# Kernel tuning notes

Hardware: AMD Instinct MI355X
Metric: run time of the kernel (lower is better)

## Reference

```python
import jax, jax.numpy as jnp
import numpy as np

B, T, C = 4, 2048, 768
H, D = 6, 128


def apply_rotary_emb(x, cos, sin):
    # x: (B, T, H, D); cos, sin: (1, T, 1, D//2)
    d = x.shape[-1] // 2
    x1, x2 = x[..., :d], x[..., d:]
    y1 = x1 * cos + x2 * sin
    y2 = -x1 * sin + x2 * cos
    return jnp.concatenate([y1, y2], axis=-1)


def rmsnorm(x):
    eps = 1e-15
    ms = jnp.mean(x * x, axis=-1, keepdims=True)
    return x / jnp.sqrt(ms + eps)


def setup_inputs() -> dict:
    key = jax.random.key(0)
    ks = jax.random.split(key, 7)
    s = 0.02
    return {
        "x": jax.random.normal(ks[0], (B, T, C), jnp.float32),
        "cos": jax.random.normal(ks[1], (1, T, 1, D // 2), jnp.float32),
        "sin": jax.random.normal(ks[2], (1, T, 1, D // 2), jnp.float32),
        "Wq": jax.random.normal(ks[3], (C, C), jnp.float32) * s,
        "Wk": jax.random.normal(ks[4], (C, C), jnp.float32) * s,
        "Wv": jax.random.normal(ks[5], (C, C), jnp.float32) * s,
        "Wo": jax.random.normal(ks[6], (C, C), jnp.float32) * s,
    }


def reference(x, cos, sin, Wq, Wk, Wv, Wo):
    b, t, c = x.shape
    # QKV projections (nn.Linear: x @ W.T)
    q = (x @ Wq.T).reshape(b, t, H, D)
    k = (x @ Wk.T).reshape(b, t, H, D)
    v = (x @ Wv.T).reshape(b, t, H, D)
    # RoPE then QK-RMSNorm
    q = rmsnorm(apply_rotary_emb(q, cos, sin))
    k = rmsnorm(apply_rotary_emb(k, cos, sin))
    # (B, H, T, D)
    q = q.transpose(0, 2, 1, 3)
    k = k.transpose(0, 2, 1, 3)
    v = v.transpose(0, 2, 1, 3)
    scores = jnp.einsum('bhqd,bhkd->bhqk', q, k) / jnp.sqrt(jnp.float32(D))
    causal = jnp.tril(jnp.ones((t, t), dtype=bool))
    scores = jnp.where(causal[None, None], scores, -jnp.inf)
    attn = jax.nn.softmax(scores, axis=-1)
    out = jnp.einsum('bhqk,bhkd->bhqd', attn, v)
    out = out.transpose(0, 2, 1, 3).reshape(b, t, c)
    return out @ Wo.T
```

## Files before the change

kernel.cpp:

```cpp
#include <hip/hip_runtime.h>

#define T_SEQ 2048
#define NH    6
#define HD    128
#define CDIM  768
#define NQKV  2304
#define MROWS 8192
#define NSLOT 1104

typedef __attribute__((ext_vector_type(8)))  short bf16x8;
typedef __attribute__((ext_vector_type(4)))  float f32x4;
typedef __attribute__((ext_vector_type(16))) float f32x16;
typedef __attribute__((ext_vector_type(2)))  int   i32x2;

__device__ __forceinline__ unsigned short f2bf(float f){
  unsigned int u = __builtin_bit_cast(unsigned int, f);
  u += 0x7fffu + ((u >> 16) & 1u);
  return (unsigned short)(u >> 16);
}
__device__ __forceinline__ float bf2f(unsigned short h){
  unsigned int u = ((unsigned int)h) << 16;
  return __builtin_bit_cast(float, u);
}
__device__ __forceinline__ unsigned int cvtpk(float lo, float hi){
  unsigned int r;
  asm("v_cvt_pk_bf16_f32 %0, %1, %2" : "=v"(r) : "v"(lo), "v"(hi));
  return r;
}

__device__ __forceinline__ void gload_lds16(const void* g, void* l){
  __builtin_amdgcn_global_load_lds(
      (const __attribute__((address_space(1))) unsigned int*)g,
      (__attribute__((address_space(3))) unsigned int*)l, 16, 0, 0);
}

__device__ __forceinline__ int ncq(int Q){
  return Q < 3 ? 1 : Q < 7 ? 2 : Q < 10 ? 3 : Q < 14 ? 4 : 5;
}
__device__ __forceinline__ int cumc(int Q){
  return Q < 4 ? Q : Q < 8 ? 3 + 2*(Q-3) : Q < 11 ? 11 + 3*(Q-7)
       : Q < 15 ? 20 + 4*(Q-10) : 36 + 5*(Q-14);
}

__global__ __launch_bounds__(256) void cvt_f32_bf16(
    const float* __restrict__ in, unsigned short* __restrict__ out, int n4){
  int i = blockIdx.x * 256 + threadIdx.x;
  if (i >= n4) return;
  float4 v = reinterpret_cast<const float4*>(in)[i];
  ushort4 o;
  o.x = f2bf(v.x); o.y = f2bf(v.y); o.z = f2bf(v.z); o.w = f2bf(v.w);
  reinterpret_cast<ushort4*>(out)[i] = o;
}

__global__ __launch_bounds__(256) void cvt_w4(
    const float* __restrict__ w0, const float* __restrict__ w1,
    const float* __restrict__ w2, const float* __restrict__ w3,
    unsigned short* __restrict__ out){
  const int which = blockIdx.y;
  const float* src = which == 0 ? w0 : which == 1 ? w1 : which == 2 ? w2 : w3;
  int i = blockIdx.x * 256 + threadIdx.x;
  float4 v = reinterpret_cast<const float4*>(src)[i];
  ushort4 o;
  o.x = f2bf(v.x); o.y = f2bf(v.y); o.z = f2bf(v.z); o.w = f2bf(v.w);
  reinterpret_cast<ushort4*>(out + (size_t)which * CDIM * CDIM)[i] = o;
}

template<int EPI>
__global__ __launch_bounds__(256) void gemm_bt(
    const unsigned short* __restrict__ A,
    const unsigned short* __restrict__ B,
    void* __restrict__ Cv, int M, int N, int K,
    const float* __restrict__ cosp, const float* __restrict__ sinp)
{
  __shared__ unsigned short As[128 * 64];
  __shared__ unsigned short Bs[128 * 64];
  const int tid  = threadIdx.x;
  const int lane = tid & 63;
  const int wave = tid >> 6;
  const int lr = lane & 15, lg = lane >> 4;
  const int srow = lane >> 3;
  const int sslot = (lane & 7) ^ (lane >> 3);
  const int gx = gridDim.x, gy = gridDim.y, nwg = gx * gy;
  const int flat = blockIdx.y * gx + blockIdx.x;
  const int nf = (flat & 7) * (nwg >> 3) + (flat >> 3);
  const int row0 = (nf / gy) * 128, col0 = (nf % gy) * 128;
  const int wrow = wave * 32;

  f32x4 acc[2][8];
  const f32x4 z = {0.f, 0.f, 0.f, 0.f};
  #pragma unroll
  for (int i = 0; i < 2; ++i)
    #pragma unroll
    for (int j = 0; j < 8; ++j) acc[i][j] = z;

  for (int k0 = 0; k0 < K; k0 += 64){
    #pragma unroll
    for (int i = 0; i < 4; ++i){
      int seg = wave * 4 + i;
      int r = seg * 8 + srow;
      gload_lds16(&A[(size_t)(row0 + r) * K + k0 + sslot * 8], &As[seg * 512]);
      gload_lds16(&B[(size_t)(col0 + r) * K + k0 + sslot * 8], &Bs[seg * 512]);
    }
    __syncthreads();
    #pragma unroll
    for (int kk = 0; kk < 64; kk += 32){
      bf16x8 af[2], bfr[8];
      #pragma unroll
      for (int mi = 0; mi < 2; ++mi)
        af[mi] = *reinterpret_cast<const bf16x8*>(
            &As[(wrow + mi*16 + lr) * 64 + ((((kk>>3) + lg) ^ (lr & 7)) * 8)]);
      #pragma unroll
      for (int ni = 0; ni < 8; ++ni)
        bfr[ni] = *reinterpret_cast<const bf16x8*>(
            &Bs[(ni*16 + lr) * 64 + ((((kk>>3) + lg) ^ (lr & 7)) * 8)]);
      #pragma unroll
      for (int mi = 0; mi < 2; ++mi)
        #pragma unroll
        for (int ni = 0; ni < 8; ++ni)
          acc[mi][ni] = __builtin_amdgcn_mfma_f32_16x16x32_bf16(af[mi], bfr[ni], acc[mi][ni], 0, 0, 0);
    }
    __syncthreads();
  }

  if (EPI == 0){
    float* Cf = reinterpret_cast<float*>(Cv);
    #pragma unroll
    for (int mi = 0; mi < 2; ++mi)
      #pragma unroll
      for (int ni = 0; ni < 8; ++ni)
        #pragma unroll
        for (int r = 0; r < 4; ++r)
          Cf[(size_t)(row0 + wrow + mi*16 + lg*4 + r) * N + col0 + ni*16 + lr] = acc[mi][ni][r];
  } else {
    unsigned short* Cb = reinterpret_cast<unsigned short*>(Cv);
    const int ct = col0 >> 7;
    if (ct >= 12){
      #pragma unroll
      for (int mi = 0; mi < 2; ++mi)
        #pragma unroll
        for (int ni = 0; ni < 8; ++ni)
          #pragma unroll
          for (int r = 0; r < 4; ++r)
            Cb[(size_t)(row0 + wrow + mi*16 + lg*4 + r) * N + col0 + ni*16 + lr] =
                f2bf(acc[mi][ni][r]);
    } else {
      #pragma unroll
      for (int mi = 0; mi < 2; ++mi){
        #pragma unroll
        for (int r = 0; r < 4; ++r){
          const int row = row0 + wrow + mi*16 + lg*4 + r;
          const int t = row & (T_SEQ - 1);
          float y1[4], y2[4], ssp = 0.f;
          #pragma unroll
          for (int ni = 0; ni < 4; ++ni){
            const int d = ni*16 + lr;
            float c = cosp[t * 64 + d];
            float s = sinp[t * 64 + d];
            float x1 = acc[mi][ni][r], x2 = acc[mi][ni+4][r];
            y1[ni] = x1 * c + x2 * s;
            y2[ni] = x2 * c - x1 * s;
            ssp += y1[ni]*y1[ni] + y2[ni]*y2[ni];
          }
          #pragma unroll
          for (int off = 1; off < 16; off <<= 1) ssp += __shfl_xor(ssp, off);
          const float inv = rsqrtf(ssp * (1.0f / 128.0f) + 1e-15f);
          #pragma unroll
          for (int ni = 0; ni < 4; ++ni){
            const int d = ni*16 + lr;
            Cb[(size_t)row * N + col0 + d]      = f2bf(y1[ni] * inv);
            Cb[(size_t)row * N + col0 + d + 64] = f2bf(y2[ni] * inv);
          }
        }
      }
    }
  }
}

__global__ __launch_bounds__(256) void transpose_v(
    const unsigned short* __restrict__ QKVb, unsigned short* __restrict__ Vt)
{
  __shared__ unsigned short tile[64][66];
  const int tid = threadIdx.x;
  const int t0  = blockIdx.x * 64;
  const int hd  = blockIdx.y;
  const int b   = blockIdx.z;
  const int h = hd >> 1, dhalf = (hd & 1) * 64;
  const unsigned short* src = QKVb + (size_t)b * T_SEQ * NQKV + 2 * CDIM + h * HD + dhalf;
  #pragma unroll
  for (int it = 0; it < 2; ++it){
    int ch = tid + it * 256;
    int r = ch >> 3, cc = (ch & 7) * 8;
    *reinterpret_cast<int4*>(&tile[r][cc]) =
        *reinterpret_cast<const int4*>(&src[(size_t)(t0 + r) * NQKV + cc]);
  }
  __syncthreads();
  unsigned short* dst = Vt + ((size_t)(b * NH + h) * HD + dhalf) * T_SEQ + t0;
  #pragma unroll
  for (int it = 0; it < 2; ++it){
    int ch = tid + it * 256;
    int d = ch >> 3, cc = (ch & 7) * 8;
    union { int4 v; unsigned short u[8]; } w;
    #pragma unroll
    for (int j = 0; j < 8; ++j) w.u[j] = tile[cc + j][d];
    *reinterpret_cast<int4*>(&dst[(size_t)d * T_SEQ + cc]) = w.v;
  }
}

__global__ __launch_bounds__(256) void attn_fwd(
    const unsigned short* __restrict__ QKVb,
    const unsigned short* __restrict__ Vt,
    unsigned short* __restrict__ AO,
    unsigned short* __restrict__ Op, float* __restrict__ Mp, float* __restrict__ Lp)
{
  __shared__ unsigned short Ks[64][136];
  __shared__ unsigned short Vs[128][72];
  const int tid = threadIdx.x;
  const int lane = tid & 63, wave = tid >> 6;
  const int l31 = lane & 31, hi = lane >> 5;

  const int flat = blockIdx.x;
  const int nf = (flat & 7) * 138 + (flat >> 3);
  const int bh = nf / 46;
  const int L = 45 - (nf % 46);
  int Q, c;
  if (L < 3)      { Q = L; c = 0; }
  else if (L < 11){ int m = L - 3;  Q = 3 + (m >> 1);  c = m & 1; }
  else if (L < 20){ int m = L - 11; Q = 7 + m / 3;     c = m % 3; }
  else if (L < 36){ int m = L - 20; Q = 10 + (m >> 2); c = m & 3; }
  else            { int m = L - 36; Q = 14 + m / 5;    c = m % 5; }
  const int nc = ncq(Q);
  const int tiles = 2 * Q + 2;
  const int base = tiles / nc, rem = tiles % nc;
  const int tbeg = c * base + (c < rem ? c : rem);
  const int tend = tbeg + base + (c < rem ? 1 : 0);
  const int b = bh / NH, h = bh % NH;
  const int qw = Q * 128 + wave * 32;

  const unsigned short* Qp = QKVb + (size_t)(b * T_SEQ) * NQKV + h * HD;
  const unsigned short* Kp = QKVb + (size_t)(b * T_SEQ) * NQKV + CDIM + h * HD;
  const unsigned short* Vp = Vt + (size_t)bh * HD * T_SEQ;

  bf16x8 qf[8];
  #pragma unroll
  for (int c4 = 0; c4 < 8; ++c4)
    qf[c4] = *reinterpret_cast<const bf16x8*>(
        &Qp[(size_t)(qw + l31) * NQKV + c4 * 16 + hi * 8]);

  f32x16 o[4];
  #pragma unroll
  for (int db = 0; db < 4; ++db)
    #pragma unroll
    for (int r = 0; r < 16; ++r) o[db][r] = 0.f;
  float mrun = -__builtin_inff(), lrun = 0.f;
  const float scl = 0.08838834764831845f;

  for (int t = tbeg; t < tend; ++t){
    const int kv0 = t * 64;
    #pragma unroll
    for (int it = 0; it < 4; ++it){
      int ch = tid + it * 256;
      int r = ch >> 4, cc = (ch & 15) * 8;
      *reinterpret_cast<int4*>(&Ks[r][cc]) =
          *reinterpret_cast<const int4*>(&Kp[(size_t)(kv0 + r) * NQKV + cc]);
      int rv = ch >> 3, cv = (ch & 7) * 8;
      *reinterpret_cast<int4*>(&Vs[rv][cv]) =
          *reinterpret_cast<const int4*>(&Vp[(size_t)rv * T_SEQ + kv0 + cv]);
    }
    __syncthreads();

    if (kv0 <= qw + 31){
      f32x16 s[2];
      #pragma unroll
      for (int r = 0; r < 16; ++r){ s[0][r] = 0.f; s[1][r] = 0.f; }
      __builtin_amdgcn_s_setprio(1);
      #pragma unroll
      for (int c4 = 0; c4 < 8; ++c4){
        bf16x8 k0 = *reinterpret_cast<const bf16x8*>(&Ks[l31][c4 * 16 + hi * 8]);
        bf16x8 k1 = *reinterpret_cast<const bf16x8*>(&Ks[32 + l31][c4 * 16 + hi * 8]);
        s[0] = __builtin_amdgcn_mfma_f32_32x32x16_bf16(k0, qf[c4], s[0], 0, 0, 0);
        s[1] = __builtin_amdgcn_mfma_f32_32x32x16_bf16(k1, qf[c4], s[1], 0, 0, 0);
      }
      __builtin_amdgcn_s_setprio(0);

      const int qg = qw + l31;
      if (kv0 + 63 > qw){
        #pragma unroll
        for (int blk = 0; blk < 2; ++blk)
          #pragma unroll
          for (int r = 0; r < 16; ++r){
            int kg = kv0 + 32 * blk + (r & 3) + 8 * (r >> 2) + 4 * hi;
            s[blk][r] = (kg <= qg) ? s[blk][r] * scl : -__builtin_inff();
          }
      } else {
        #pragma unroll
        for (int blk = 0; blk < 2; ++blk)
          #pragma unroll
          for (int r = 0; r < 16; ++r) s[blk][r] *= scl;
      }

      float t8[8];
      #pragma unroll
      for (int blk = 0; blk < 2; ++blk)
        #pragma unroll
        for (int j = 0; j < 4; ++j)
          t8[blk * 4 + j] = fmaxf(fmaxf(s[blk][4*j], s[blk][4*j+1]),
                                  fmaxf(s[blk][4*j+2], s[blk][4*j+3]));
      float pm = fmaxf(fmaxf(fmaxf(t8[0], t8[1]), fmaxf(t8[2], t8[3])),
                       fmaxf(fmaxf(t8[4], t8[5]), fmaxf(t8[6], t8[7])));
      pm = fmaxf(pm, __shfl_xor(pm, 32));

      if (__any(pm > mrun)){
        float mn = fmaxf(mrun, pm);
        float scf = (mrun == -__builtin_inff()) ? 0.f : __expf(mrun - mn);
        mrun = mn; lrun *= scf;
        #pragma unroll
        for (int r = 0; r < 16; ++r){
          float scr = __shfl(scf, (r & 3) + 8 * (r >> 2) + 4 * hi, 32);
          #pragma unroll
          for (int db = 0; db < 4; ++db) o[db][r] *= scr;
        }
      }

      float a8[8];
      #pragma unroll
      for (int blk = 0; blk < 2; ++blk)
        #pragma unroll
        for (int j = 0; j < 4; ++j){
          float p0 = __expf(s[blk][4*j]   - mrun);
          float p1 = __expf(s[blk][4*j+1] - mrun);
          float p2 = __expf(s[blk][4*j+2] - mrun);
          float p3 = __expf(s[blk][4*j+3] - mrun);
          s[blk][4*j] = p0; s[blk][4*j+1] = p1; s[blk][4*j+2] = p2; s[blk][4*j+3] = p3;
          a8[blk * 4 + j] = (p0 + p1) + (p2 + p3);
        }
      float ls = ((a8[0] + a8[1]) + (a8[2] + a8[3])) + ((a8[4] + a8[5]) + (a8[6] + a8[7]));
      lrun += ls + __shfl_xor(ls, 32);

      __builtin_amdgcn_s_setprio(1);
      #pragma unroll
      for (int kc = 0; kc < 4; ++kc){
        const int blk = kc >> 1, base2 = (kc & 1) * 8;
        unsigned int a0 = cvtpk(s[blk][base2+0], s[blk][base2+1]);
        unsigned int b0 = cvtpk(s[blk][base2+4], s[blk][base2+5]);
        unsigned int a1 = cvtpk(s[blk][base2+2], s[blk][base2+3]);
        unsigned int b1 = cvtpk(s[blk][base2+6], s[blk][base2+7]);
        i32x2 sw0 = __builtin_amdgcn_permlane32_swap((int)a0, (int)b0, false, false);
        i32x2 sw1 = __builtin_amdgcn_permlane32_swap((int)a1, (int)b1, false, false);
        union { bf16x8 v; unsigned int u[4]; } pa;
        pa.u[0] = (unsigned int)sw0[0];
        pa.u[1] = (unsigned int)sw1[0];
        pa.u[2] = (unsigned int)sw0[1];
        pa.u[3] = (unsigned int)sw1[1];
        #pragma unroll
        for (int db = 0; db < 4; ++db){
          bf16x8 vf = *reinterpret_cast<const bf16x8*>(
              &Vs[db * 32 + l31][kc * 16 + hi * 8]);
          o[db] = __builtin_amdgcn_mfma_f32_32x32x16_bf16(pa.v, vf, o[db], 0, 0, 0);
        }
      }
      __builtin_amdgcn_s_setprio(0);
    }
    __syncthreads();
  }

  if (nc == 1){
    float inv = 1.0f / lrun;
    #pragma unroll
    for (int r = 0; r < 16; ++r){
      const int crow = (r & 3) + 8 * (r >> 2) + 4 * hi;
      float ir = __shfl(inv, crow, 32);
      #pragma unroll
      for (int db = 0; db < 4; ++db)
        AO[((size_t)b * T_SEQ + qw + crow) * CDIM + h * HD + db * 32 + l31] =
            f2bf(o[db][r] * ir);
    }
  } else {
    const int slot = bh * 46 + cumc(Q) + c;
    unsigned short* OpW = Op + (size_t)slot * 128 * 128;
    #pragma unroll
    for (int r = 0; r < 16; ++r){
      const int row = wave * 32 + (r & 3) + 8 * (r >> 2) + 4 * hi;
      #pragma unroll
      for (int db = 0; db < 4; ++db)
        OpW[row * 128 + db * 32 + l31] = f2bf(o[db][r]);
    }
    if (hi == 0){
      Mp[(size_t)slot * 128 + wave * 32 + l31] = mrun;
      Lp[(size_t)slot * 128 + wave * 32 + l31] = lrun;
    }
  }
}

__global__ __launch_bounds__(256) void attn_combine(
    const unsigned short* __restrict__ Op, const float* __restrict__ Mp,
    const float* __restrict__ Lp, unsigned short* __restrict__ AO)
{
  const int Q  = 3 + blockIdx.x;
  const int bh = blockIdx.y;
  const int b = bh / NH, h = bh % NH;
  const int nc = ncq(Q);
  const int slot0 = bh * 46 + cumc(Q);
  #pragma unroll
  for (int u = 0; u < 16; ++u){
    int unit = threadIdx.x + u * 256;
    int r = unit >> 5, d4 = unit & 31;
    float m = -__builtin_inff();
    for (int cc = 0; cc < nc; ++cc)
      m = fmaxf(m, Mp[(size_t)(slot0 + cc) * 128 + r]);
    float l = 0.f;
    float a0 = 0.f, a1 = 0.f, a2 = 0.f, a3 = 0.f;
    for (int cc = 0; cc < nc; ++cc){
      float w = __expf(Mp[(size_t)(slot0 + cc) * 128 + r] - m);
      l += w * Lp[(size_t)(slot0 + cc) * 128 + r];
      const ushort4 v = *reinterpret_cast<const ushort4*>(
          &Op[((size_t)(slot0 + cc) * 128 + r) * 128 + d4 * 4]);
      a0 += w * bf2f(v.x); a1 += w * bf2f(v.y);
      a2 += w * bf2f(v.z); a3 += w * bf2f(v.w);
    }
    float inv = 1.0f / l;
    ushort4 ov;
    ov.x = f2bf(a0 * inv); ov.y = f2bf(a1 * inv);
    ov.z = f2bf(a2 * inv); ov.w = f2bf(a3 * inv);
    *reinterpret_cast<ushort4*>(
        &AO[((size_t)b * T_SEQ + Q * 128 + r) * CDIM + h * HD + d4 * 4]) = ov;
  }
}

extern "C" void kernel_launch(void* const* d_in, const int* in_sizes, int n_in,
                              void* d_out, int out_size, void* d_ws, size_t ws_size,
                              hipStream_t stream)
{
  (void)in_sizes; (void)n_in; (void)out_size; (void)ws_size;
  const float* x    = (const float*)d_in[0];
  const float* cosp = (const float*)d_in[1];
  const float* sinp = (const float*)d_in[2];
  const float* Wq   = (const float*)d_in[3];
  const float* Wk   = (const float*)d_in[4];
  const float* Wv   = (const float*)d_in[5];
  const float* Wo   = (const float*)d_in[6];
  float* out = (float*)d_out;

  unsigned short* xb    = (unsigned short*)d_ws;
  unsigned short* Wqkvb = xb    + (size_t)MROWS * CDIM;
  unsigned short* Wob   = Wqkvb + (size_t)NQKV * CDIM;
  unsigned short* QKVb  = Wob   + (size_t)CDIM * CDIM;
  unsigned short* Vtb   = QKVb  + (size_t)MROWS * NQKV;
  unsigned short* AO    = Vtb   + (size_t)MROWS * CDIM;
  unsigned short* Op    = AO    + (size_t)MROWS * CDIM;
  float* Mp = (float*)(Op + (size_t)NSLOT * 128 * 128);
  float* Lp = Mp + (size_t)NSLOT * 128;

  int n4x = MROWS * CDIM / 4;
  cvt_f32_bf16<<<(n4x + 255) / 256, 256, 0, stream>>>(x, xb, n4x);
  cvt_w4<<<dim3(CDIM * CDIM / 4 / 256, 4), 256, 0, stream>>>(Wq, Wk, Wv, Wo, Wqkvb);

  gemm_bt<1><<<dim3(MROWS / 128, NQKV / 128), 256, 0, stream>>>(
      xb, Wqkvb, QKVb, MROWS, NQKV, CDIM, cosp, sinp);
  transpose_v<<<dim3(T_SEQ / 64, 12, 4), 256, 0, stream>>>(QKVb, Vtb);
  attn_fwd<<<NSLOT, 256, 0, stream>>>(QKVb, Vtb, AO, Op, Mp, Lp);
  attn_combine<<<dim3(13, 24), 256, 0, stream>>>(Op, Mp, Lp, AO);
  gemm_bt<0><<<dim3(MROWS / 128, CDIM / 128), 256, 0, stream>>>(
      AO, Wob, out, MROWS, CDIM, CDIM, nullptr, nullptr);
}
```

Before: 214.5 us.

## Shrink attention query tile to 64 rows with 2-wave blocks and re-split schedule

Halves the attention query block from 128 to 64 rows, using 128-thread blocks (two waves) instead of four, and rebuilds the causal split-KV schedule with 90 work units per head and 2160 blocks. The aim is finer granularity and better load balance and occupancy across CUs, with less wasted work on the diagonal. In exchange, each K/V tile loaded into shared memory serves half as many query rows, so K/V traffic roughly doubles, and the combine kernel has more partial slots to merge.

```diff
diff --git a/kernel.cpp b/kernel.cpp
--- a/kernel.cpp
+++ b/kernel.cpp
@@ -6,7 +6,7 @@
 #define CDIM  768
 #define NQKV  2304
 #define MROWS 8192
-#define NSLOT 1104
+#define NSLOT 2160
 
 typedef __attribute__((ext_vector_type(8)))  short bf16x8;
 typedef __attribute__((ext_vector_type(4)))  float f32x4;
@@ -34,12 +34,12 @@
       (__attribute__((address_space(3))) unsigned int*)l, 16, 0, 0);
 }
 
-__device__ __forceinline__ int ncq(int Q){
-  return Q < 3 ? 1 : Q < 7 ? 2 : Q < 10 ? 3 : Q < 14 ? 4 : 5;
-}
-__device__ __forceinline__ int cumc(int Q){
-  return Q < 4 ? Q : Q < 8 ? 3 + 2*(Q-3) : Q < 11 ? 11 + 3*(Q-7)
-       : Q < 15 ? 20 + 4*(Q-10) : 36 + 5*(Q-14);
+__device__ __forceinline__ int ncq(int q){
+  return q < 7 ? 1 : q < 14 ? 2 : q < 21 ? 3 : q < 28 ? 4 : 5;
+}
+__device__ __forceinline__ int cumc(int q){
+  return q < 7 ? q : q < 14 ? 7 + 2*(q-7) : q < 21 ? 21 + 3*(q-14)
+       : q < 28 ? 42 + 4*(q-21) : 70 + 5*(q-28);
 }
 
 __global__ __launch_bounds__(256) void cvt_f32_bf16(
@@ -206,7 +206,7 @@
   }
 }
 
-__global__ __launch_bounds__(256) void attn_fwd(
+__global__ __launch_bounds__(128) void attn_fwd(
     const unsigned short* __restrict__ QKVb,
     const unsigned short* __restrict__ Vt,
     unsigned short* __restrict__ AO,
@@ -219,22 +219,22 @@
   const int l31 = lane & 31, hi = lane >> 5;
 
   const int flat = blockIdx.x;
-  const int nf = (flat & 7) * 138 + (flat >> 3);
-  const int bh = nf / 46;
-  const int L = 45 - (nf % 46);
-  int Q, c;
-  if (L < 3)      { Q = L; c = 0; }
-  else if (L < 11){ int m = L - 3;  Q = 3 + (m >> 1);  c = m & 1; }
-  else if (L < 20){ int m = L - 11; Q = 7 + m / 3;     c = m % 3; }
-  else if (L < 36){ int m = L - 20; Q = 10 + (m >> 2); c = m & 3; }
-  else            { int m = L - 36; Q = 14 + m / 5;    c = m % 5; }
-  const int nc = ncq(Q);
-  const int tiles = 2 * Q + 2;
+  const int nf = (flat & 7) * 270 + (flat >> 3);
+  const int bh = nf / 90;
+  const int L = 89 - (nf % 90);
+  int q, c;
+  if (L < 7)      { q = L; c = 0; }
+  else if (L < 21){ int m = L - 7;  q = 7 + (m >> 1);  c = m & 1; }
+  else if (L < 42){ int m = L - 21; q = 14 + m / 3;    c = m % 3; }
+  else if (L < 70){ int m = L - 42; q = 21 + (m >> 2); c = m & 3; }
+  else            { int m = L - 70; q = 28 + m / 5;    c = m % 5; }
+  const int nc = ncq(q);
+  const int tiles = q + 1;
   const int base = tiles / nc, rem = tiles % nc;
   const int tbeg = c * base + (c < rem ? c : rem);
   const int tend = tbeg + base + (c < rem ? 1 : 0);
   const int b = bh / NH, h = bh % NH;
-  const int qw = Q * 128 + wave * 32;
+  const int qw = q * 64 + wave * 32;
 
   const unsigned short* Qp = QKVb + (size_t)(b * T_SEQ) * NQKV + h * HD;
   const unsigned short* Kp = QKVb + (size_t)(b * T_SEQ) * NQKV + CDIM + h * HD;
@@ -257,8 +257,8 @@
   for (int t = tbeg; t < tend; ++t){
     const int kv0 = t * 64;
     #pragma unroll
-    for (int it = 0; it < 4; ++it){
-      int ch = tid + it * 256;
+    for (int it = 0; it < 8; ++it){
+      int ch = tid + it * 128;
       int r = ch >> 4, cc = (ch & 15) * 8;
       *reinterpret_cast<int4*>(&Ks[r][cc]) =
           *reinterpret_cast<const int4*>(&Kp[(size_t)(kv0 + r) * NQKV + cc]);
@@ -375,8 +375,8 @@
             f2bf(o[db][r] * ir);
     }
   } else {
-    const int slot = bh * 46 + cumc(Q) + c;
-    unsigned short* OpW = Op + (size_t)slot * 128 * 128;
+    const int slot = bh * 90 + cumc(q) + c;
+    unsigned short* OpW = Op + (size_t)slot * 64 * 128;
     #pragma unroll
     for (int r = 0; r < 16; ++r){
       const int row = wave * 32 + (r & 3) + 8 * (r >> 2) + 4 * hi;
@@ -385,8 +385,8 @@
         OpW[row * 128 + db * 32 + l31] = f2bf(o[db][r]);
     }
     if (hi == 0){
-      Mp[(size_t)slot * 128 + wave * 32 + l31] = mrun;
-      Lp[(size_t)slot * 128 + wave * 32 + l31] = lrun;
+      Mp[(size_t)slot * 64 + wave * 32 + l31] = mrun;
+      Lp[(size_t)slot * 64 + wave * 32 + l31] = lrun;
     }
   }
 }
@@ -395,25 +395,25 @@
     const unsigned short* __restrict__ Op, const float* __restrict__ Mp,
     const float* __restrict__ Lp, unsigned short* __restrict__ AO)
 {
-  const int Q  = 3 + blockIdx.x;
+  const int q  = 7 + blockIdx.x;
   const int bh = blockIdx.y;
   const int b = bh / NH, h = bh % NH;
-  const int nc = ncq(Q);
-  const int slot0 = bh * 46 + cumc(Q);
-  #pragma unroll
-  for (int u = 0; u < 16; ++u){
+  const int nc = ncq(q);
+  const int slot0 = bh * 90 + cumc(q);
+  #pragma unroll
+  for (int u = 0; u < 8; ++u){
     int unit = threadIdx.x + u * 256;
     int r = unit >> 5, d4 = unit & 31;
     float m = -__builtin_inff();
     for (int cc = 0; cc < nc; ++cc)
-      m = fmaxf(m, Mp[(size_t)(slot0 + cc) * 128 + r]);
+      m = fmaxf(m, Mp[(size_t)(slot0 + cc) * 64 + r]);
     float l = 0.f;
     float a0 = 0.f, a1 = 0.f, a2 = 0.f, a3 = 0.f;
     for (int cc = 0; cc < nc; ++cc){
-      float w = __expf(Mp[(size_t)(slot0 + cc) * 128 + r] - m);
-      l += w * Lp[(size_t)(slot0 + cc) * 128 + r];
+      float w = __expf(Mp[(size_t)(slot0 + cc) * 64 + r] - m);
+      l += w * Lp[(size_t)(slot0 + cc) * 64 + r];
       const ushort4 v = *reinterpret_cast<const ushort4*>(
-          &Op[((size_t)(slot0 + cc) * 128 + r) * 128 + d4 * 4]);
+          &Op[((size_t)(slot0 + cc) * 64 + r) * 128 + d4 * 4]);
       a0 += w * bf2f(v.x); a1 += w * bf2f(v.y);
       a2 += w * bf2f(v.z); a3 += w * bf2f(v.w);
     }
@@ -422,7 +422,7 @@
     ov.x = f2bf(a0 * inv); ov.y = f2bf(a1 * inv);
     ov.z = f2bf(a2 * inv); ov.w = f2bf(a3 * inv);
     *reinterpret_cast<ushort4*>(
-        &AO[((size_t)b * T_SEQ + Q * 128 + r) * CDIM + h * HD + d4 * 4]) = ov;
+        &AO[((size_t)b * T_SEQ + q * 64 + r) * CDIM + h * HD + d4 * 4]) = ov;
   }
 }
 
@@ -447,8 +447,8 @@
   unsigned short* Vtb   = QKVb  + (size_t)MROWS * NQKV;
   unsigned short* AO    = Vtb   + (size_t)MROWS * CDIM;
   unsigned short* Op    = AO    + (size_t)MROWS * CDIM;
-  float* Mp = (float*)(Op + (size_t)NSLOT * 128 * 128);
-  float* Lp = Mp + (size_t)NSLOT * 128;
+  float* Mp = (float*)(Op + (size_t)NSLOT * 64 * 128);
+  float* Lp = Mp + (size_t)NSLOT * 64;
 
   int n4x = MROWS * CDIM / 4;
   cvt_f32_bf16<<<(n4x + 255) / 256, 256, 0, stream>>>(x, xb, n4x);
@@ -457,8 +457,8 @@
   gemm_bt<1><<<dim3(MROWS / 128, NQKV / 128), 256, 0, stream>>>(
       xb, Wqkvb, QKVb, MROWS, NQKV, CDIM, cosp, sinp);
   transpose_v<<<dim3(T_SEQ / 64, 12, 4), 256, 0, stream>>>(QKVb, Vtb);
-  attn_fwd<<<NSLOT, 256, 0, stream>>>(QKVb, Vtb, AO, Op, Mp, Lp);
-  attn_combine<<<dim3(13, 24), 256, 0, stream>>>(Op, Mp, Lp, AO);
+  attn_fwd<<<NSLOT, 128, 0, stream>>>(QKVb, Vtb, AO, Op, Mp, Lp);
+  attn_combine<<<dim3(25, 24), 256, 0, stream>>>(Op, Mp, Lp, AO);
   gemm_bt<0><<<dim3(MROWS / 128, CDIM / 128), 256, 0, stream>>>(
       AO, Wob, out, MROWS, CDIM, CDIM, nullptr, nullptr);
 }
```

New measurement: 261.1 us. 1.22x slower.
